# Kernel optimization log

Measured on AMD Instinct MI355X. Metric: run time of the kernel, lower is better.

The kernel has to match this reference:

```python
import jax, jax.numpy as jnp
import numpy as np

B, L, D, H, K = 4, 2048, 1024, 16, 3
HEAD_DIM = D // H
LN_EPS = 1e-5


def setup_inputs() -> dict:
    key = jax.random.key(0)
    ks = jax.random.split(key, 12)
    w = lambda k, shp: jax.random.normal(k, shp, jnp.float32) * (shp[-1] ** -0.5)
    return {
        "x": jax.random.normal(ks[0], (B, L, D), jnp.float32),
        "band_importance": jax.random.normal(ks[1], (1, L), jnp.float32) * 0.02,
        "Wq": w(ks[2], (D, D)), "bq": jnp.zeros((D,), jnp.float32),
        "Wk": w(ks[3], (D, D)), "bk": jnp.zeros((D,), jnp.float32),
        "Wv": w(ks[4], (D, D)), "bv": jnp.zeros((D,), jnp.float32),
        "Wo": w(ks[5], (D, D)), "bo": jnp.zeros((D,), jnp.float32),
        "gamma": jnp.ones((D,), jnp.float32),
        "beta": jnp.zeros((D,), jnp.float32),
    }


def reference(x, band_importance, Wq, bq, Wk, bk, Wv, bv, Wo, bo, gamma, beta):
    Bx, Lx, Dx = x.shape
    hd = Dx // H
    # top-k over softmax(band_importance); PyTorch bool attn_mask: True = BLOCKED
    imp = jax.nn.softmax(band_importance, axis=-1)[0]            # (L,)
    _, idx = jax.lax.top_k(imp, K)                               # (K,) int
    col_mask = jnp.zeros((Lx,), bool).at[idx].set(True)          # (L,) True -> masked out
    bias = jnp.where(col_mask, -jnp.inf, 0.0).astype(x.dtype)    # (L,)

    q = (x @ Wq.T + bq).reshape(Bx, Lx, H, hd)
    k_ = (x @ Wk.T + bk).reshape(Bx, Lx, H, hd)
    v = (x @ Wv.T + bv).reshape(Bx, Lx, H, hd)

    scale = 1.0 / np.sqrt(hd)
    scores = jnp.einsum("bqhd,bkhd->bhqk", q, k_) * scale + bias[None, None, None, :]
    attn = jax.nn.softmax(scores, axis=-1)                       # (B,H,L,L)
    ctx = jnp.einsum("bhqk,bkhd->bqhd", attn, v).reshape(Bx, Lx, Dx)
    attn_out = ctx @ Wo.T + bo

    y = x + attn_out                                             # residual
    mu = jnp.mean(y, axis=-1, keepdims=True)
    var = jnp.mean((y - mu) ** 2, axis=-1, keepdims=True)
    return (y - mu) * jax.lax.rsqrt(var + LN_EPS) * gamma + beta
```

## Files before the change

kernel.cpp:

```cpp
#include <hip/hip_runtime.h>

#define GAS __attribute__((address_space(1)))
#define LAS __attribute__((address_space(3)))

typedef __attribute__((ext_vector_type(8))) short short8;
typedef __attribute__((ext_vector_type(4))) float f32x4;
typedef __attribute__((ext_vector_type(16))) float f32x16;
typedef __attribute__((ext_vector_type(4))) unsigned int u32x4;

#define MFMA16(a,b,c) __builtin_amdgcn_mfma_f32_16x16x32_bf16(a,b,c,0,0,0)
#define MFMA32(a,b,c) __builtin_amdgcn_mfma_f32_32x32x16_bf16(a,b,c,0,0,0)

__device__ __forceinline__ unsigned short f2b(float f) {
  unsigned u = __float_as_uint(f);
  u += 0x7fffu + ((u >> 16) & 1u);
  return (unsigned short)(u >> 16);
}
__device__ __forceinline__ float b2f(unsigned short h) {
  return __uint_as_float(((unsigned)h) << 16);
}
__device__ __forceinline__ unsigned cvtpk(float a, float b) {
  unsigned r;
  asm("v_cvt_pk_bf16_f32 %0, %1, %2" : "=v"(r) : "v"(a), "v"(b));
  return r;
}
__device__ __forceinline__ void pl32swap(unsigned &x, unsigned &y) {
  auto r = __builtin_amdgcn_permlane32_swap((int)x, (int)y, false, false);
  x = (unsigned)r[0]; y = (unsigned)r[1];
}
__device__ __forceinline__ float xhalf_sum(float v) {
  auto r = __builtin_amdgcn_permlane32_swap(__float_as_int(v), __float_as_int(v), false, false);
  return __int_as_float(r[0]) + __int_as_float(r[1]);
}
__device__ __forceinline__ float fexp2(float x) {
  float r;
  asm("v_exp_f32 %0, %1" : "=v"(r) : "v"(x));
  return r;
}
__device__ __forceinline__ short8 ld8(const unsigned short* p) {
  return *reinterpret_cast<const short8*>(p);
}

union FW { u32x4 u; short8 s; };

__global__ void cvt_topk(const float* __restrict__ x,
                         const float* __restrict__ Wq, const float* __restrict__ Wk,
                         const float* __restrict__ Wv, const float* __restrict__ Wo,
                         const float* __restrict__ band,
                         unsigned short* __restrict__ xb,
                         unsigned short* __restrict__ Wqkvb,
                         unsigned short* __restrict__ Wob,
                         int* __restrict__ idxout) {
  const int bid = blockIdx.x;
  if (bid < 12288) {
    const float* src;
    unsigned short* dst;
    int idx;
    if (bid < 8192) {
      src = x; dst = xb; idx = bid * 256 + threadIdx.x;
    } else {
      int wb = bid - 8192;
      int seg = wb >> 10;
      idx = (wb & 1023) * 256 + threadIdx.x;
      src = (seg == 0) ? Wq : (seg == 1) ? Wk : (seg == 2) ? Wv : Wo;
      dst = (seg == 3) ? Wob : (Wqkvb + (size_t)seg * 1048576);
    }
    float4 v = reinterpret_cast<const float4*>(src)[idx];
    ushort4 o;
    o.x = f2b(v.x); o.y = f2b(v.y); o.z = f2b(v.z); o.w = f2b(v.w);
    reinterpret_cast<ushort4*>(dst)[idx] = o;
    return;
  }
  __shared__ float svals[256];
  __shared__ int   sidx[256];
  __shared__ int   chosen[3];
  const int t = threadIdx.x;
  for (int pass = 0; pass < 3; ++pass) {
    float best = -INFINITY; int bi = 1 << 30;
    for (int j = t; j < 2048; j += 256) {
      float v = band[j];
      bool skip = false;
      for (int p2 = 0; p2 < pass; ++p2) skip |= (chosen[p2] == j);
      if (!skip && (v > best || (v == best && j < bi))) { best = v; bi = j; }
    }
    svals[t] = best; sidx[t] = bi;
    __syncthreads();
    for (int s = 128; s > 0; s >>= 1) {
      if (t < s) {
        float v2 = svals[t + s]; int i2 = sidx[t + s];
        if (v2 > svals[t] || (v2 == svals[t] && i2 < sidx[t])) { svals[t] = v2; sidx[t] = i2; }
      }
      __syncthreads();
    }
    if (t == 0) chosen[pass] = sidx[0];
    __syncthreads();
  }
  if (t < 3) idxout[t] = chosen[t];
}

__global__ __launch_bounds__(512, 1) void gemm_qkv256(
    const unsigned short* __restrict__ A,
    const unsigned short* __restrict__ Wqkv,
    const float* __restrict__ bq, const float* __restrict__ bk,
    const float* __restrict__ bv,
    unsigned short* __restrict__ qout, unsigned short* __restrict__ kout,
    unsigned short* __restrict__ vtout, float qscale)
{
  __shared__ short Ls[3][2][8192];
  const int tid = threadIdx.x;
  const int w = tid >> 6, lane = tid & 63;
  const int wm = w >> 2, wn = w & 3;
  const int flat = blockIdx.y * 32 + blockIdx.x;
  const int swb = (flat & 7) * 48 + (flat >> 3);
  const int m0 = (swb & 31) * 256, n0 = (swb >> 5) * 256;

  const int seg = n0 >> 10;
  const float* biasp = (seg == 0) ? bq : (seg == 1) ? bk : bv;
  const float scale = (seg == 0) ? qscale : 1.0f;

  f32x4 acc[8][4];
  #pragma unroll
  for (int mt = 0; mt < 8; ++mt)
    #pragma unroll
    for (int nt = 0; nt < 4; ++nt)
      #pragma unroll
      for (int r = 0; r < 4; ++r) acc[mt][nt][r] = 0.f;

  const int srow = tid >> 2;
  const int scol = ((tid & 3) ^ ((srow >> 2) & 3)) * 8;
  const unsigned short* ap = A + (size_t)(m0 + srow) * 1024 + scol;
  const unsigned short* bp = Wqkv + (size_t)(n0 + srow) * 1024 + scol;
  const int ldst = tid * 8;

#define STG_A0(bufi, tt) __builtin_amdgcn_global_load_lds(                     \
    (const GAS void*)(ap + (size_t)(tt) * 32), (LAS void*)&Ls[bufi][0][ldst], 16, 0, 0)
#define STG_A1(bufi, tt) __builtin_amdgcn_global_load_lds(                     \
    (const GAS void*)(ap + (size_t)(tt) * 32 + 131072), (LAS void*)&Ls[bufi][0][4096 + ldst], 16, 0, 0)
#define STG_B0(bufi, tt) __builtin_amdgcn_global_load_lds(                     \
    (const GAS void*)(bp + (size_t)(tt) * 32), (LAS void*)&Ls[bufi][1][ldst], 16, 0, 0)
#define STG_B1(bufi, tt) __builtin_amdgcn_global_load_lds(                     \
    (const GAS void*)(bp + (size_t)(tt) * 32 + 131072), (LAS void*)&Ls[bufi][1][4096 + ldst], 16, 0, 0)

  const int r15 = lane & 15;
  const int fcol = ((lane >> 4) * 8) ^ (((r15 >> 2) & 3) << 3);
  const int arow0 = wm * 128 + r15;
  const int brow0 = wn * 64 + r15;

  STG_A0(0, 0); STG_A1(0, 0); STG_B0(0, 0); STG_B1(0, 0);
  STG_A0(1, 1); STG_A1(1, 1); STG_B0(1, 1); STG_B1(1, 1);

  for (int t = 0; t < 32; ++t) {
    if (t < 31) { asm volatile("s_waitcnt vmcnt(4)" ::: "memory"); }
    else        { asm volatile("s_waitcnt vmcnt(0)" ::: "memory"); }
    __builtin_amdgcn_sched_barrier(0);
    __builtin_amdgcn_s_barrier();
    __builtin_amdgcn_sched_barrier(0);
    const int buf = t % 3;
    const int sbuf = (t + 2) % 3;
    const short* Ab = &Ls[buf][0][0];
    const short* Bb = &Ls[buf][1][0];

    short8 bf[4];
    #pragma unroll
    for (int nt = 0; nt < 4; ++nt)
      bf[nt] = *reinterpret_cast<const short8*>(&Bb[(brow0 + nt * 16) * 32 + fcol]);

    #pragma unroll
    for (int ph = 0; ph < 4; ++ph) {
      if (t < 30) {
        if (ph == 0) STG_A0(sbuf, t + 2);
        else if (ph == 1) STG_A1(sbuf, t + 2);
        else if (ph == 2) STG_B0(sbuf, t + 2);
        else STG_B1(sbuf, t + 2);
      }
      short8 a0 = *reinterpret_cast<const short8*>(&Ab[(arow0 + (ph * 2) * 16) * 32 + fcol]);
      short8 a1 = *reinterpret_cast<const short8*>(&Ab[(arow0 + (ph * 2 + 1) * 16) * 32 + fcol]);
      __builtin_amdgcn_s_setprio(1);
      #pragma unroll
      for (int nt = 0; nt < 4; ++nt) {
        acc[ph * 2][nt] = MFMA16(a0, bf[nt], acc[ph * 2][nt]);
        acc[ph * 2 + 1][nt] = MFMA16(a1, bf[nt], acc[ph * 2 + 1][nt]);
      }
      __builtin_amdgcn_s_setprio(0);
    }

    asm volatile("s_waitcnt lgkmcnt(0)" ::: "memory");
    __builtin_amdgcn_sched_barrier(0);
  }

  if (seg == 2) {
    #pragma unroll
    for (int nt = 0; nt < 4; ++nt) {
      int coll = (n0 + wn * 64 + nt * 16 + r15) & 1023;
      float bval = biasp[coll];
      int h_ = coll >> 6, d_ = coll & 63;
      #pragma unroll
      for (int mt = 0; mt < 8; ++mt) {
        int rbase = m0 + wm * 128 + mt * 16 + ((lane >> 4) << 2);
        int b_ = rbase >> 11, lt_ = rbase & 2047;
        ushort4 pk;
        pk.x = f2b(acc[mt][nt][0] + bval);
        pk.y = f2b(acc[mt][nt][1] + bval);
        pk.z = f2b(acc[mt][nt][2] + bval);
        pk.w = f2b(acc[mt][nt][3] + bval);
        *reinterpret_cast<ushort4*>(
            &vtout[(((size_t)(b_ * 16 + h_)) * 64 + d_) * 2048 + lt_]) = pk;
      }
    }
  } else {
    unsigned short* outp = (seg == 0) ? qout : kout;
    #pragma unroll
    for (int nt = 0; nt < 4; ++nt) {
      int coll = (n0 + wn * 64 + nt * 16 + r15) & 1023;
      float bval = biasp[coll];
      int h_ = coll >> 6, d_ = coll & 63;
      #pragma unroll
      for (int mt = 0; mt < 8; ++mt) {
        int rbase = m0 + wm * 128 + mt * 16 + ((lane >> 4) << 2);
        #pragma unroll
        for (int r = 0; r < 4; ++r) {
          unsigned short val = f2b((acc[mt][nt][r] + bval) * scale);
          int row = rbase + r;
          int b_ = row >> 11, lt_ = row & 2047;
          outp[(((size_t)(b_ * 16 + h_)) * 2048 + lt_) * 64 + d_] = val;
        }
      }
    }
  }
}

__global__ __launch_bounds__(256) void gemm_wo(
    const unsigned short* __restrict__ A,
    const unsigned short* __restrict__ Bw,
    const float* __restrict__ bias,
    unsigned short* __restrict__ C)
{
  __shared__ short As[128][64];
  __shared__ short Bs[128][64];
  const int tid = threadIdx.x;
  const int w = tid >> 6, lane = tid & 63;
  const int wm = w >> 1, wn = w & 1;
  const int flat = blockIdx.y * 64 + blockIdx.x;
  const int swb = (flat & 7) * 64 + (flat >> 3);
  const int m0 = (swb & 63) * 128, n0 = (swb >> 6) * 128;
  const int rA = lane >> 3, cA = lane & 7;

  f32x4 acc[4][4];
  #pragma unroll
  for (int mt = 0; mt < 4; ++mt)
    #pragma unroll
    for (int nt = 0; nt < 4; ++nt)
      #pragma unroll
      for (int r = 0; r < 4; ++r) acc[mt][nt][r] = 0.f;

  for (int kt = 0; kt < 16; ++kt) {
    #pragma unroll
    for (int j = 0; j < 4; ++j) {
      int r = w * 32 + j * 8;
      const unsigned short* ga = A + (size_t)(m0 + r + rA) * 1024 + kt * 64 + cA * 8;
      __builtin_amdgcn_global_load_lds((const GAS void*)ga, (LAS void*)&As[r][0], 16, 0, 0);
      const unsigned short* gb = Bw + (size_t)(n0 + r + rA) * 1024 + kt * 64 + cA * 8;
      __builtin_amdgcn_global_load_lds((const GAS void*)gb, (LAS void*)&Bs[r][0], 16, 0, 0);
    }
    __syncthreads();
    #pragma unroll
    for (int kc = 0; kc < 2; ++kc) {
      short8 a[4], b[4];
      #pragma unroll
      for (int mt = 0; mt < 4; ++mt)
        a[mt] = *reinterpret_cast<const short8*>(
            &As[wm * 64 + mt * 16 + (lane & 15)][kc * 32 + (lane >> 4) * 8]);
      #pragma unroll
      for (int nt = 0; nt < 4; ++nt)
        b[nt] = *reinterpret_cast<const short8*>(
            &Bs[wn * 64 + nt * 16 + (lane & 15)][kc * 32 + (lane >> 4) * 8]);
      __builtin_amdgcn_s_setprio(1);
      #pragma unroll
      for (int mt = 0; mt < 4; ++mt)
        #pragma unroll
        for (int nt = 0; nt < 4; ++nt)
          acc[mt][nt] = MFMA16(a[mt], b[nt], acc[mt][nt]);
      __builtin_amdgcn_s_setprio(0);
    }
    __syncthreads();
  }
  #pragma unroll
  for (int nt = 0; nt < 4; ++nt) {
    int col = n0 + wn * 64 + nt * 16 + (lane & 15);
    float bval = bias[col];
    #pragma unroll
    for (int mt = 0; mt < 4; ++mt) {
      int rbase = m0 + wm * 64 + mt * 16 + ((lane >> 4) << 2);
      #pragma unroll
      for (int r = 0; r < 4; ++r)
        C[(size_t)(rbase + r) * 1024 + col] = f2b(acc[mt][nt][r] + bval);
    }
  }
}

#define PACK8(S, j0, OUT) {                                        \
    unsigned A_ = cvtpk(S[(j0)+0], S[(j0)+1]);                     \
    unsigned B_ = cvtpk(S[(j0)+4], S[(j0)+5]);                     \
    unsigned C_ = cvtpk(S[(j0)+2], S[(j0)+3]);                     \
    unsigned D_ = cvtpk(S[(j0)+6], S[(j0)+7]);                     \
    pl32swap(A_, B_); pl32swap(C_, D_);                            \
    FW f_; f_.u[0] = A_; f_.u[1] = C_; f_.u[2] = B_; f_.u[3] = D_; \
    OUT = f_.s; }

__global__ __launch_bounds__(256, 3) void attn4(
    const unsigned short* __restrict__ qg,
    const unsigned short* __restrict__ kg,
    const unsigned short* __restrict__ vtg,
    const int* __restrict__ midx,
    unsigned short* __restrict__ ctx)
{
  __shared__ short Ks[2][64 * 64];
  __shared__ short Vs[2][64 * 64];
  const int tid = threadIdx.x, w = tid >> 6, lane = tid & 63;
  const int flat = blockIdx.y * 16 + blockIdx.x;
  const int swzb = (flat & 7) * 128 + (flat >> 3);
  const int qt = swzb & 15, bh = swzb >> 4;
  const int q0 = qt * 128;
  const int lo5 = lane & 31, hi = lane >> 5;
  const int i0 = midx[0], i1 = midx[1], i2 = midx[2];

  const int qrow = q0 + w * 32 + lo5;
  const unsigned short* qp = qg + ((size_t)bh * 2048 + qrow) * 64 + hi * 8;
  short8 qf[4];
  #pragma unroll
  for (int ds = 0; ds < 4; ++ds) qf[ds] = ld8(qp + ds * 16);

  f32x16 oacc0, oacc1, lacc;
  #pragma unroll
  for (int r = 0; r < 16; ++r) { oacc0[r] = 0.f; oacc1[r] = 0.f; lacc[r] = 0.f; }

  const int swzoff = (((lane & 7) ^ (lane >> 3))) * 8;
  const unsigned short* kp0 =
      kg + ((size_t)bh * 2048 + w * 8 + (lane >> 3)) * 64 + swzoff;
  const unsigned short* kp1 = kp0 + 32 * 64;
  const unsigned short* vp0 =
      vtg + ((size_t)(bh * 64 + w * 8 + (lane >> 3))) * 2048 + swzoff;
  const unsigned short* vp1 = vp0 + 32 * 2048;

#define STAGE_K(bufi, tt) do {                                                 \
    __builtin_amdgcn_global_load_lds((const GAS void*)(kp0 + (tt) * 4096),     \
        (LAS void*)&Ks[bufi][(w * 8) * 64], 16, 0, 0);                         \
    __builtin_amdgcn_global_load_lds((const GAS void*)(kp1 + (tt) * 4096),     \
        (LAS void*)&Ks[bufi][(32 + w * 8) * 64], 16, 0, 0);                    \
  } while (0)
#define STAGE_V(bufi, tt) do {                                                 \
    __builtin_amdgcn_global_load_lds((const GAS void*)(vp0 + (tt) * 64),       \
        (LAS void*)&Vs[bufi][(w * 8) * 64], 16, 0, 0);                         \
    __builtin_amdgcn_global_load_lds((const GAS void*)(vp1 + (tt) * 64),       \
        (LAS void*)&Vs[bufi][(32 + w * 8) * 64], 16, 0, 0);                    \
  } while (0)

  STAGE_K(0, 0); STAGE_V(0, 0);
  STAGE_K(1, 1); STAGE_V(1, 1);

  for (int t = 0; t < 32; ++t) {
    const int buf = t & 1;
    if (t < 31) { asm volatile("s_waitcnt vmcnt(4)" ::: "memory"); }
    else        { asm volatile("s_waitcnt vmcnt(0)" ::: "memory"); }
    __builtin_amdgcn_sched_barrier(0);
    __builtin_amdgcn_s_barrier();
    __builtin_amdgcn_sched_barrier(0);

    short8 kf[8];
    #pragma unroll
    for (int ds = 0; ds < 4; ++ds) {
      int cw = ds * 2 + hi;
      kf[2 * ds] = *reinterpret_cast<const short8*>(
          &Ks[buf][lo5 * 64 + ((cw ^ (lo5 & 7)) * 8)]);
      kf[2 * ds + 1] = *reinterpret_cast<const short8*>(
          &Ks[buf][(32 + lo5) * 64 + ((cw ^ (lo5 & 7)) * 8)]);
    }
    asm volatile("s_waitcnt lgkmcnt(0)" ::: "memory");
    __builtin_amdgcn_sched_barrier(0);
    __builtin_amdgcn_s_barrier();
    __builtin_amdgcn_sched_barrier(0);
    if (t < 30) STAGE_K(buf, t + 2);

    f32x16 s0, s1;
    #pragma unroll
    for (int r = 0; r < 16; ++r) { s0[r] = 0.f; s1[r] = 0.f; }
    __builtin_amdgcn_s_setprio(1);
    #pragma unroll
    for (int ds = 0; ds < 4; ++ds) {
      s0 = MFMA32(kf[2 * ds], qf[ds], s0);
      s1 = MFMA32(kf[2 * ds + 1], qf[ds], s1);
    }
    __builtin_amdgcn_s_setprio(0);

    #pragma unroll
    for (int r = 0; r < 16; ++r) s0[r] = fexp2(s0[r]);
    #pragma unroll
    for (int r = 0; r < 16; ++r) s1[r] = fexp2(s1[r]);

    int t64 = t * 64;
    bool tm = ((unsigned)(i0 - t64) < 64u) | ((unsigned)(i1 - t64) < 64u) |
              ((unsigned)(i2 - t64) < 64u);
    if (tm) {
      #pragma unroll
      for (int r = 0; r < 16; ++r) {
        int kg0 = t64 + (r & 3) + 8 * (r >> 2) + 4 * hi;
        int kg1 = kg0 + 32;
        if (kg0 == i0 || kg0 == i1 || kg0 == i2) s0[r] = 0.f;
        if (kg1 == i0 || kg1 == i1 || kg1 == i2) s1[r] = 0.f;
      }
    }

    #pragma unroll
    for (int r = 0; r < 16; ++r) lacc[r] += s0[r] + s1[r];

    short8 pa[4];
    PACK8(s0, 0, pa[0]); PACK8(s0, 8, pa[1]);
    PACK8(s1, 0, pa[2]); PACK8(s1, 8, pa[3]);

    short8 vf[8];
    #pragma unroll
    for (int ks = 0; ks < 4; ++ks) {
      int cw = ks * 2 + hi;
      vf[2 * ks] = *reinterpret_cast<const short8*>(
          &Vs[buf][lo5 * 64 + ((cw ^ (lo5 & 7)) * 8)]);
      vf[2 * ks + 1] = *reinterpret_cast<const short8*>(
          &Vs[buf][(32 + lo5) * 64 + ((cw ^ (lo5 & 7)) * 8)]);
    }
    asm volatile("s_waitcnt lgkmcnt(0)" ::: "memory");
    __builtin_amdgcn_sched_barrier(0);
    __builtin_amdgcn_s_barrier();
    __builtin_amdgcn_sched_barrier(0);
    if (t < 30) STAGE_V(buf, t + 2);

    __builtin_amdgcn_s_setprio(1);
    #pragma unroll
    for (int ks = 0; ks < 4; ++ks) {
      oacc0 = MFMA32(pa[ks], vf[2 * ks], oacc0);
      oacc1 = MFMA32(pa[ks], vf[2 * ks + 1], oacc1);
    }
    __builtin_amdgcn_s_setprio(0);
  }

  float lsum = 0.f;
  #pragma unroll
  for (int r = 0; r < 16; ++r) lsum += lacc[r];
  lsum = xhalf_sum(lsum);
  const int bb = bh >> 4, hh = bh & 15;
  float rinv = 1.0f / lsum;
  #pragma unroll
  for (int r = 0; r < 16; ++r) {
    int row = (r & 3) + 8 * (r >> 2) + 4 * hi;
    float rv = __int_as_float(__builtin_amdgcn_ds_bpermute(
        (row + (lane & 32)) * 4, __float_as_int(rinv)));
    int qr = q0 + w * 32 + row;
    size_t base = (((size_t)(bb * 2048 + qr)) * 16 + hh) * 64;
    ctx[base + lo5]      = f2b(oacc0[r] * rv);
    ctx[base + 32 + lo5] = f2b(oacc1[r] * rv);
  }
}

__global__ __launch_bounds__(256) void resid_ln(
    const float* __restrict__ x, const unsigned short* __restrict__ ao,
    const float* __restrict__ gamma, const float* __restrict__ beta,
    float* __restrict__ out)
{
  const int row = blockIdx.x, t = threadIdx.x;
  const size_t base = (size_t)row * 1024;
  float4 xv = reinterpret_cast<const float4*>(x + base)[t];
  ushort4 av = reinterpret_cast<const ushort4*>(ao + base)[t];
  float y[4] = {xv.x + b2f(av.x), xv.y + b2f(av.y), xv.z + b2f(av.z), xv.w + b2f(av.w)};
  float sum = y[0] + y[1] + y[2] + y[3];
  float sq = y[0] * y[0] + y[1] * y[1] + y[2] * y[2] + y[3] * y[3];
  #pragma unroll
  for (int off = 1; off < 64; off <<= 1) {
    sum += __shfl_xor(sum, off);
    sq += __shfl_xor(sq, off);
  }
  __shared__ float s1[4], s2[4];
  int w = t >> 6, lane = t & 63;
  if (lane == 0) { s1[w] = sum; s2[w] = sq; }
  __syncthreads();
  sum = s1[0] + s1[1] + s1[2] + s1[3];
  sq = s2[0] + s2[1] + s2[2] + s2[3];
  float mu = sum * (1.f / 1024.f);
  float var = sq * (1.f / 1024.f) - mu * mu;
  float inv = rsqrtf(var + 1e-5f);
  float4 gv = reinterpret_cast<const float4*>(gamma)[t];
  float4 bv = reinterpret_cast<const float4*>(beta)[t];
  float4 o;
  o.x = (y[0] - mu) * inv * gv.x + bv.x;
  o.y = (y[1] - mu) * inv * gv.y + bv.y;
  o.z = (y[2] - mu) * inv * gv.z + bv.z;
  o.w = (y[3] - mu) * inv * gv.w + bv.w;
  reinterpret_cast<float4*>(out + base)[t] = o;
}

extern "C" void kernel_launch(void* const* d_in, const int* in_sizes, int n_in,
                              void* d_out, int out_size, void* d_ws, size_t ws_size,
                              hipStream_t stream)
{
  const float* x     = (const float*)d_in[0];
  const float* band  = (const float*)d_in[1];
  const float* Wq    = (const float*)d_in[2];
  const float* bq    = (const float*)d_in[3];
  const float* Wk    = (const float*)d_in[4];
  const float* bk    = (const float*)d_in[5];
  const float* Wv    = (const float*)d_in[6];
  const float* bv    = (const float*)d_in[7];
  const float* Wo    = (const float*)d_in[8];
  const float* bo    = (const float*)d_in[9];
  const float* gamma = (const float*)d_in[10];
  const float* beta  = (const float*)d_in[11];
  float* out = (float*)d_out;

  char* ws = (char*)d_ws;
  int*            idxw  = (int*)(ws);
  unsigned short* xb    = (unsigned short*)(ws + 4096);
  unsigned short* Wqkvb = (unsigned short*)(ws + 16781312);
  unsigned short* Wob   = (unsigned short*)(ws + 23072768);
  unsigned short* qb    = (unsigned short*)(ws + 25169920);
  unsigned short* kb    = (unsigned short*)(ws + 41947136);
  unsigned short* ctxb  = (unsigned short*)(ws + 58724352);
  unsigned short* vtb   = (unsigned short*)(ws + 75501568);
  unsigned short* aob   = qb;

  const float QSCALE = 0.125f * 1.44269504f;

  cvt_topk<<<12289, 256, 0, stream>>>(x, Wq, Wk, Wv, Wo, band, xb, Wqkvb, Wob, idxw);

  gemm_qkv256<<<dim3(32, 12), 512, 0, stream>>>(xb, Wqkvb, bq, bk, bv,
                                                qb, kb, vtb, QSCALE);

  attn4<<<dim3(16, 64), 256, 0, stream>>>(qb, kb, vtb, idxw, ctxb);

  gemm_wo<<<dim3(64, 8), 256, 0, stream>>>(ctxb, Wob, bo, aob);

  resid_ln<<<8192, 256, 0, stream>>>(x, aob, gamma, beta, out);
}
```

Measured before the change: 226.4 us.

## Use 8-wave attention blocks sharing K/V tiles and merge barriers

The attention kernel now runs 512 threads per block covering 256 query rows instead of 256 threads covering 128, so each staged K/V tile in LDS is reused by twice as many waves. With eight waves, K and V staging becomes a single global-to-LDS load per thread into a combined STAGE8. The separate barrier before K restaging is removed, V fragment loads move earlier, and both tiles are refilled after one barrier. This halves redundant K/V global traffic and cuts barriers per iteration. The cost is more waves syncing at each barrier and K reloads now waiting behind the P·V phase.

```diff
diff --git a/kernel.cpp b/kernel.cpp
--- a/kernel.cpp
+++ b/kernel.cpp
@@ -307,7 +307,7 @@
     FW f_; f_.u[0] = A_; f_.u[1] = C_; f_.u[2] = B_; f_.u[3] = D_; \
     OUT = f_.s; }
 
-__global__ __launch_bounds__(256, 3) void attn4(
+__global__ __launch_bounds__(512, 4) void attn8(
     const unsigned short* __restrict__ qg,
     const unsigned short* __restrict__ kg,
     const unsigned short* __restrict__ vtg,
@@ -317,10 +317,10 @@
   __shared__ short Ks[2][64 * 64];
   __shared__ short Vs[2][64 * 64];
   const int tid = threadIdx.x, w = tid >> 6, lane = tid & 63;
-  const int flat = blockIdx.y * 16 + blockIdx.x;
-  const int swzb = (flat & 7) * 128 + (flat >> 3);
-  const int qt = swzb & 15, bh = swzb >> 4;
-  const int q0 = qt * 128;
+  const int flat = blockIdx.y * 8 + blockIdx.x;
+  const int swzb = (flat & 7) * 64 + (flat >> 3);
+  const int qt = swzb & 7, bh = swzb >> 3;
+  const int q0 = qt * 256;
   const int lo5 = lane & 31, hi = lane >> 5;
   const int i0 = midx[0], i1 = midx[1], i2 = midx[2];
 
@@ -334,33 +334,24 @@
   #pragma unroll
   for (int r = 0; r < 16; ++r) { oacc0[r] = 0.f; oacc1[r] = 0.f; lacc[r] = 0.f; }
 
-  const int swzoff = (((lane & 7) ^ (lane >> 3))) * 8;
-  const unsigned short* kp0 =
-      kg + ((size_t)bh * 2048 + w * 8 + (lane >> 3)) * 64 + swzoff;
-  const unsigned short* kp1 = kp0 + 32 * 64;
-  const unsigned short* vp0 =
-      vtg + ((size_t)(bh * 64 + w * 8 + (lane >> 3))) * 2048 + swzoff;
-  const unsigned short* vp1 = vp0 + 32 * 2048;
-
-#define STAGE_K(bufi, tt) do {                                                 \
-    __builtin_amdgcn_global_load_lds((const GAS void*)(kp0 + (tt) * 4096),     \
-        (LAS void*)&Ks[bufi][(w * 8) * 64], 16, 0, 0);                         \
-    __builtin_amdgcn_global_load_lds((const GAS void*)(kp1 + (tt) * 4096),     \
-        (LAS void*)&Ks[bufi][(32 + w * 8) * 64], 16, 0, 0);                    \
+  const int srow = tid >> 3;
+  const int swzoff = (((tid & 7) ^ (srow & 7))) * 8;
+  const unsigned short* kp = kg + ((size_t)bh * 2048 + srow) * 64 + swzoff;
+  const unsigned short* vp = vtg + ((size_t)bh * 64 + srow) * 2048 + swzoff;
+
+#define STAGE8(bufi, tt) do {                                                  \
+    __builtin_amdgcn_global_load_lds((const GAS void*)(kp + (size_t)(tt) * 4096), \
+        (LAS void*)&Ks[bufi][w * 512], 16, 0, 0);                              \
+    __builtin_amdgcn_global_load_lds((const GAS void*)(vp + (tt) * 64),        \
+        (LAS void*)&Vs[bufi][w * 512], 16, 0, 0);                              \
   } while (0)
-#define STAGE_V(bufi, tt) do {                                                 \
-    __builtin_amdgcn_global_load_lds((const GAS void*)(vp0 + (tt) * 64),       \
-        (LAS void*)&Vs[bufi][(w * 8) * 64], 16, 0, 0);                         \
-    __builtin_amdgcn_global_load_lds((const GAS void*)(vp1 + (tt) * 64),       \
-        (LAS void*)&Vs[bufi][(32 + w * 8) * 64], 16, 0, 0);                    \
-  } while (0)
-
-  STAGE_K(0, 0); STAGE_V(0, 0);
-  STAGE_K(1, 1); STAGE_V(1, 1);
+
+  STAGE8(0, 0);
+  STAGE8(1, 1);
 
   for (int t = 0; t < 32; ++t) {
     const int buf = t & 1;
-    if (t < 31) { asm volatile("s_waitcnt vmcnt(4)" ::: "memory"); }
+    if (t < 31) { asm volatile("s_waitcnt vmcnt(2)" ::: "memory"); }
     else        { asm volatile("s_waitcnt vmcnt(0)" ::: "memory"); }
     __builtin_amdgcn_sched_barrier(0);
     __builtin_amdgcn_s_barrier();
@@ -375,11 +366,6 @@
       kf[2 * ds + 1] = *reinterpret_cast<const short8*>(
           &Ks[buf][(32 + lo5) * 64 + ((cw ^ (lo5 & 7)) * 8)]);
     }
-    asm volatile("s_waitcnt lgkmcnt(0)" ::: "memory");
-    __builtin_amdgcn_sched_barrier(0);
-    __builtin_amdgcn_s_barrier();
-    __builtin_amdgcn_sched_barrier(0);
-    if (t < 30) STAGE_K(buf, t + 2);
 
     f32x16 s0, s1;
     #pragma unroll
@@ -391,6 +377,16 @@
       s1 = MFMA32(kf[2 * ds + 1], qf[ds], s1);
     }
     __builtin_amdgcn_s_setprio(0);
+
+    short8 vf[8];
+    #pragma unroll
+    for (int ks = 0; ks < 4; ++ks) {
+      int cw = ks * 2 + hi;
+      vf[2 * ks] = *reinterpret_cast<const short8*>(
+          &Vs[buf][lo5 * 64 + ((cw ^ (lo5 & 7)) * 8)]);
+      vf[2 * ks + 1] = *reinterpret_cast<const short8*>(
+          &Vs[buf][(32 + lo5) * 64 + ((cw ^ (lo5 & 7)) * 8)]);
+    }
 
     #pragma unroll
     for (int r = 0; r < 16; ++r) s0[r] = fexp2(s0[r]);
@@ -417,20 +413,11 @@
     PACK8(s0, 0, pa[0]); PACK8(s0, 8, pa[1]);
     PACK8(s1, 0, pa[2]); PACK8(s1, 8, pa[3]);
 
-    short8 vf[8];
-    #pragma unroll
-    for (int ks = 0; ks < 4; ++ks) {
-      int cw = ks * 2 + hi;
-      vf[2 * ks] = *reinterpret_cast<const short8*>(
-          &Vs[buf][lo5 * 64 + ((cw ^ (lo5 & 7)) * 8)]);
-      vf[2 * ks + 1] = *reinterpret_cast<const short8*>(
-          &Vs[buf][(32 + lo5) * 64 + ((cw ^ (lo5 & 7)) * 8)]);
-    }
     asm volatile("s_waitcnt lgkmcnt(0)" ::: "memory");
     __builtin_amdgcn_sched_barrier(0);
     __builtin_amdgcn_s_barrier();
     __builtin_amdgcn_sched_barrier(0);
-    if (t < 30) STAGE_V(buf, t + 2);
+    if (t < 30) STAGE8(buf, t + 2);
 
     __builtin_amdgcn_s_setprio(1);
     #pragma unroll
@@ -531,7 +518,7 @@
   gemm_qkv256<<<dim3(32, 12), 512, 0, stream>>>(xb, Wqkvb, bq, bk, bv,
                                                 qb, kb, vtb, QSCALE);
 
-  attn4<<<dim3(16, 64), 256, 0, stream>>>(qb, kb, vtb, idxw, ctxb);
+  attn8<<<dim3(8, 64), 512, 0, stream>>>(qb, kb, vtb, idxw, ctxb);
 
   gemm_wo<<<dim3(64, 8), 256, 0, stream>>>(ctxb, Wob, bo, aob);
 
```

After: 369.1 us. 1.63x slower.
